# Performance work log

Hardware: AMD Instinct MI355X
Metric: run time of the kernel (lower is better)

The kernel has to match this reference:

```python
import jax, jax.numpy as jnp
import numpy as np

B = 32768   # batch
F = 32      # per-node feature dim
H = 256     # hidden width
M = 4       # modules per node
OUT = 8     # final output dim
INIT_W = 0.003
B_INIT = 0.1


def _lin(k, din, dout):
    # fanin_init-style uniform weights, bias filled with 0.1 (hidden layers)
    s = 1.0 / np.sqrt(din)
    W = jax.random.uniform(k, (M, din, dout), jnp.float32, -s, s)
    b = jnp.full((M, dout), B_INIT, jnp.float32)
    return W, b


def setup_inputs() -> dict:
    key = jax.random.key(0)
    ks = jax.random.split(key, 16)
    feats = jax.random.normal(ks[0], (B, 4 * F), jnp.float32)
    idx = jax.random.randint(ks[1], (B, 4), 0, M)
    onehots = jax.nn.one_hot(idx, M, dtype=jnp.float32).reshape(B, 4 * M)
    input_val = jnp.concatenate([feats, onehots], axis=1)  # [B,144]

    W00, b00 = _lin(ks[2], F, H)        # node0 post layer 0
    W01, b01 = _lin(ks[3], H, H)        # node0 post layer 1
    Wpre1, bpre1 = _lin(ks[4], F, H)    # node1 pre
    Wpost1, bpost1 = _lin(ks[5], 2 * H, H)  # node1 interface (prev 256 + own 256)
    Wpre2, bpre2 = _lin(ks[6], F, H)
    Wpost2, bpost2 = _lin(ks[7], 2 * H, H)
    Wpre3, bpre3 = _lin(ks[8], F, H)
    Wpost3, bpost3 = _lin(ks[9], 2 * H, H)
    # final output layer: uniform(-init_w, init_w) for W and b, identity act
    Wfin3 = jax.random.uniform(ks[10], (M, H, OUT), jnp.float32, -INIT_W, INIT_W)
    bfin3 = jax.random.uniform(ks[11], (M, OUT), jnp.float32, -INIT_W, INIT_W)
    return dict(input_val=input_val,
                W00=W00, b00=b00, W01=W01, b01=b01,
                Wpre1=Wpre1, bpre1=bpre1, Wpost1=Wpost1, bpost1=bpost1,
                Wpre2=Wpre2, bpre2=bpre2, Wpost2=Wpost2, bpost2=bpost2,
                Wpre3=Wpre3, bpre3=bpre3, Wpost3=Wpost3, bpost3=bpost3,
                Wfin3=Wfin3, bfin3=bfin3)


def _select(h, onehot):
    # per-row pick of the assigned module's output: [B,M,D],[B,M] -> [B,D]
    return jnp.einsum('bmo,bm->bo', h, onehot)


def reference(input_val, W00, b00, W01, b01,
              Wpre1, bpre1, Wpost1, bpost1,
              Wpre2, bpre2, Wpost2, bpost2,
              Wpre3, bpre3, Wpost3, bpost3,
              Wfin3, bfin3):
    feat = lambda j: input_val[:, j * F:(j + 1) * F]
    oh = lambda j: input_val[:, 4 * F + j * M: 4 * F + (j + 1) * M]

    # node 0: two hidden layers, module-dispatched (dense-all-modules + one-hot combine)
    h = jax.nn.relu(jnp.einsum('bi,mio->bmo', feat(0), W00) + b00)
    h = jax.nn.relu(jnp.einsum('bmi,mio->bmo', h, W01) + b01)
    x = _select(h, oh(0))  # [B,H]

    def node(x_prev, fj, ohj, Wpre, bpre, Wpost, bpost):
        hp = jax.nn.relu(jnp.einsum('bi,mio->bmo', fj, Wpre) + bpre)
        # interface layer consumes concat([x_prev, hp]); split the weight to
        # avoid materializing [B,M,2H]
        hq = jax.nn.relu(jnp.einsum('bi,mio->bmo', x_prev, Wpost[:, :H, :])
                         + jnp.einsum('bmi,mio->bmo', hp, Wpost[:, H:, :])
                         + bpost)
        return hq  # [B,M,H]

    x = _select(node(x, feat(1), oh(1), Wpre1, bpre1, Wpost1, bpost1), oh(1))
    x = _select(node(x, feat(2), oh(2), Wpre2, bpre2, Wpost2, bpost2), oh(2))

    h3 = node(x, feat(3), oh(3), Wpre3, bpre3, Wpost3, bpost3)  # [B,M,H]
    out = jnp.einsum('bmi,mio->bmo', h3, Wfin3) + bfin3          # final linear, identity act
    return _select(out, oh(3))  # [B,OUT]
```

## Files before the change

### kernel.cpp

```cpp
#include <hip/hip_runtime.h>

#define NB 32768
#define MAXTILE 768
#define ROWS 64
#define NT 4
#define XHS 536

typedef short s8v __attribute__((ext_vector_type(8)));
typedef short s4v __attribute__((ext_vector_type(4)));
typedef float f4v __attribute__((ext_vector_type(4)));
typedef unsigned short u16;
typedef unsigned short u16x4 __attribute__((ext_vector_type(4)));
typedef unsigned int u32;
typedef unsigned char u8;

__device__ __forceinline__ float bf2f(u16 u) { return __uint_as_float(((u32)u) << 16); }
__device__ __forceinline__ u16 f2bf(float f) {
    u32 x = __float_as_uint(f);
    x += 0x7FFFu + ((x >> 16) & 1u);
    return (u16)(x >> 16);
}
__device__ __forceinline__ s8v ld8(const u16* p) { return *reinterpret_cast<const s8v*>(p); }

#define MFMA16(a, b, c) __builtin_amdgcn_mfma_f32_16x16x32_bf16((a), (b), (c), 0, 0, 0)

template <int N> struct IC { static constexpr int v = N; };

__device__ __forceinline__ void detect_flag(const void* input, int tid, int* shflag)
{
    if (tid < 64) {
        u32 w = ((const u32*)input)[tid];
        u32 h0 = w & 0xFFFFu;
        u32 e0 = (h0 >> 7) & 0xFFu;
        bool plaus = (h0 == 0u) || (e0 >= 96u && e0 <= 143u);
        unsigned long long m = __ballot(plaus);
        if (tid == 0) *shflag = (__popcll(m) >= 48) ? 1 : 0;
    }
}

struct RepArgs {
    const void* W01; const void* Wp[3]; const void* pre[4]; const void* fin;
    const void* bias[9];
    u16 *rPre, *rW01, *rWp[3], *rFin, *cbias;
};

__global__ __launch_bounds__(256) void prepA_kernel(const void* __restrict__ inputv,
                                                    int* __restrict__ histT,
                                                    u16* __restrict__ keyloc,
                                                    RepArgs R)
{
    __shared__ int lcnt[256];
    __shared__ u16 T[2048];
    __shared__ int shmisc;
    int tid = threadIdx.x;
    int b = blockIdx.x;
    detect_flag(inputv, tid, &shmisc);
    __syncthreads();
    int flag = shmisc;

    if (b < 128) {
        lcnt[tid] = 0;
        __syncthreads();
        int row = (b << 8) + tid;
        const u32* in32 = (const u32*)inputv;
        const u16* in16 = (const u16*)inputv;
        int key = 0;
#pragma unroll
        for (int j = 0; j < 4; j++) {
            int base = row * 144 + 128 + j * 4;
            u32 v1, v2, v3;
            if (flag) { v1 = in16[base + 1]; v2 = in16[base + 2]; v3 = in16[base + 3]; }
            else      { v1 = in32[base + 1]; v2 = in32[base + 2]; v3 = in32[base + 3]; }
            int m = v1 ? 1 : (v2 ? 2 : (v3 ? 3 : 0));
            key |= m << (j << 1);
        }
        int loc = atomicAdd(&lcnt[key], 1);
        keyloc[row] = (u16)(key | (loc << 8));
        __syncthreads();
        histT[tid * 128 + b] = lcnt[tid];
        return;
    }

    int rb = b - 128;
    const void* src; u16* dst; int K, k0, mrow, kq;
    if (rb < 128) {
        int tile = rb >> 2; kq = rb & 3;
        int m = tile >> 3, s = tile & 7;
        src = R.W01; dst = R.rW01 + (m * 8 + s) * 8192; K = 256; k0 = s * 32; mrow = m;
    } else if (rb < 896) {
        int u = rb - 128, mat = u >> 8, r = u & 255;
        int tile = r >> 2; kq = r & 3;
        int m = tile >> 4, s = tile & 15;
        src = R.Wp[mat]; dst = R.rWp[mat] + (m * 16 + s) * 8192; K = 512; k0 = s * 32; mrow = m;
    } else if (rb < 960) {
        int u = rb - 896;
        int tile = u >> 2; kq = u & 3;
        int mat = tile >> 2, m = tile & 3;
        src = R.pre[mat]; dst = R.rPre + (mat * 4 + m) * 8192; K = 32; k0 = 0; mrow = m;
    } else if (rb < 964) {
        int m = rb - 960;
        const u16* s16 = (const u16*)R.fin;
        const float* s32 = (const float*)R.fin;
        u16* d = R.rFin + m * 4096;
        for (int half = 0; half < 2; half++) {
            for (int i = tid; i < 1024; i += 256) {
                int kk = half * 128 + (i >> 3);
                T[i] = flag ? s16[(m * 256 + kk) * 8 + (i & 7)]
                            : f2bf(s32[(m * 256 + kk) * 8 + (i & 7)]);
            }
            __syncthreads();
            for (int i = tid; i < 2048; i += 256) {
                int s = (half << 2) + (i >> 9), lane = (i >> 3) & 63, j = i & 7;
                int q = lane >> 4, l16 = lane & 15;
                int k = s * 32 + q * 8 + j;
                d[s * 512 + lane * 8 + j] = (l16 < 8) ? T[(k - half * 128) * 8 + l16] : (u16)0;
            }
            __syncthreads();
        }
        return;
    } else {
        const int sz[9] = {1024,1024,1024,1024,1024,1024,1024,1024,32};
        const int of[9] = {0,1024,2048,3072,4096,5120,6144,7168,8192};
        for (int i = tid; i < 8224; i += 256) {
            int t = i, e = 0;
            while (t >= sz[e]) { t -= sz[e]; e++; }
            R.cbias[of[e] + t] = flag ? ((const u16*)R.bias[e])[t]
                                      : f2bf(((const float*)R.bias[e])[t]);
        }
        return;
    }
    const u16* s16 = (const u16*)src;
    const float* s32 = (const float*)src;
    for (int i = tid; i < 2048; i += 256) {
        int kk = i >> 8, n = i & 255;
        int srcIdx = (mrow * K + k0 + kq * 8 + kk) * 256 + n;
        T[i] = flag ? s16[srcIdx] : f2bf(s32[srcIdx]);
    }
    __syncthreads();
    for (int i = tid; i < 2048; i += 256) {
        int mt = i >> 7, r = i & 127, l15 = r >> 3, j = i & 7;
        dst[mt * 512 + kq * 128 + r] = T[j * 256 + mt * 16 + l15];
    }
}

__global__ __launch_bounds__(256) void scatter_kernel(const int* __restrict__ histT,
                                                      const u16* __restrict__ keyloc,
                                                      int* __restrict__ perm,
                                                      int4* __restrict__ tileInfo)
{
    __shared__ int lcnt[256];
    __shared__ int sBase[256];
    int tid = threadIdx.x;
    int b = blockIdx.x;

    const int4* hrow = (const int4*)(histT + tid * 128);
    int tot = 0, before = 0;
#pragma unroll
    for (int j = 0; j < 32; j++) {
        int4 h = hrow[j];
        int i4 = j << 2;
        tot += h.x + h.y + h.z + h.w;
        if (i4 + 0 < b) before += h.x;
        if (i4 + 1 < b) before += h.y;
        if (i4 + 2 < b) before += h.z;
        if (i4 + 3 < b) before += h.w;
    }
    lcnt[tid] = tot;
    __syncthreads();
    for (int off = 1; off < 256; off <<= 1) {
        int v = (tid >= off) ? lcnt[tid - off] : 0;
        __syncthreads();
        lcnt[tid] += v;
        __syncthreads();
    }
    int gbase = lcnt[tid] - tot;
    sBase[tid] = gbase + before;
    __syncthreads();

    if (b == 0) {
        int tiles = (tot + ROWS - 1) / ROWS;
        lcnt[tid] = tiles;
        __syncthreads();
        for (int off = 1; off < 256; off <<= 1) {
            int v = (tid >= off) ? lcnt[tid - off] : 0;
            __syncthreads();
            lcnt[tid] += v;
            __syncthreads();
        }
        int tbase = lcnt[tid] - tiles;
        int ttot = lcnt[255];
        for (int t = 0; t < tiles; t++) {
            int rem = tot - t * ROWS;
            tileInfo[tbase + t] = make_int4(tid, gbase + t * ROWS, rem > ROWS ? ROWS : rem, 0);
        }
        for (int i = ttot + tid; i < MAXTILE; i += 256)
            tileInfo[i] = make_int4(0, 0, 0, 0);
    }

    int row = (b << 8) + tid;
    u32 kl = keyloc[row];
    int key = kl & 255, loc = kl >> 8;
    perm[sBase[key] + loc] = row;
}

struct MainP { const u16 *rPre, *rW01, *rWp1, *rWp2, *rWp3, *rFin, *cbias; };

__global__ __launch_bounds__(1024, 8) void main_kernel(
    const void* __restrict__ inRaw,
    const int* __restrict__ perm, const int4* __restrict__ tileInfo,
    MainP P, void* __restrict__ outp)
{
    __shared__ __align__(16) u16 xh[ROWS * XHS];
    __shared__ int rowids[ROWS];
    __shared__ int shflag;

    int tid = threadIdx.x;
    int lane = tid & 63, w = tid >> 6, quad = lane >> 4, l16 = lane & 15;

    int4 ti = tileInfo[blockIdx.x];
    int key = ti.x, ppos = ti.y, cntIn = ti.z;
    if (cntIn <= 0) return;

    detect_flag(inRaw, tid, &shflag);
    if (tid < ROWS) {
        int g = tid < cntIn ? tid : cntIn - 1;
        rowids[tid] = perm[ppos + g];
    }
    __syncthreads();
    int flag = shflag;
    int rows_[NT];
#pragma unroll
    for (int nt = 0; nt < NT; nt++) rows_[nt] = rowids[nt * 16 + l16];

    const u16* in16 = (const u16*)inRaw;
    const float* in32 = (const float*)inRaw;
    int mt = w;

    f4v acc[NT];
    s8v fb[NT];

    auto gemm_run = [&](auto nc, const u16* Ab, int ks0) {
        constexpr int N = decltype(nc)::v;
        constexpr int D = 3;
        const u16* base = Ab + mt * 512 + lane * 8;
        s8v A[D];
#pragma unroll
        for (int d = 0; d < D && d < N; d++) A[d] = ld8(base + d * 8192);
        __syncthreads();
#pragma unroll
        for (int s = 0; s < N; s++) {
            s8v c = A[s % D];
            if (s + D < N) A[s % D] = ld8(base + (s + D) * 8192);
#pragma unroll
            for (int nt = 0; nt < NT; nt++) {
                s8v B = ld8(&xh[(nt * 16 + l16) * XHS + (ks0 + s) * 32 + quad * 8]);
                acc[nt] = MFMA16(c, B, acc[nt]);
            }
        }
    };

    for (int node = 0; node < 4; node++) {
        int m = (key >> (node << 1)) & 3;

#pragma unroll
        for (int nt = 0; nt < NT; nt++) {
            int off = rows_[nt] * 144 + (node << 5) + (quad << 3);
            if (flag) fb[nt] = ld8(in16 + off);
            else {
                f4v f0 = *(const f4v*)(in32 + off);
                f4v f1 = *(const f4v*)(in32 + off + 4);
                s8v r;
#pragma unroll
                for (int j = 0; j < 4; j++) { r[j] = (short)f2bf(f0[j]); r[4 + j] = (short)f2bf(f1[j]); }
                fb[nt] = r;
            }
        }

        {
            const u16* preB = P.rPre + ((node << 2) + m) * 8192;
            s8v a = ld8(preB + mt * 512 + lane * 8);
            u16x4 bv = *(const u16x4*)(P.cbias + node * 2048 + m * 256 + mt * 16 + quad * 4);
            f4v bias;
#pragma unroll
            for (int r = 0; r < 4; r++) bias[r] = bf2f(bv[r]);
#pragma unroll
            for (int nt = 0; nt < NT; nt++) {
                f4v c = MFMA16(a, fb[nt], bias);
                s4v p;
#pragma unroll
                for (int r = 0; r < 4; r++) { float v = c[r] > 0.f ? c[r] : 0.f; p[r] = (short)f2bf(v); }
                *(s4v*)&xh[(nt * 16 + l16) * XHS + 256 + mt * 16 + quad * 4] = p;
            }
        }

        {
            u16x4 bv = *(const u16x4*)(P.cbias + node * 2048 + 1024 + m * 256 + mt * 16 + quad * 4);
            f4v f0;
#pragma unroll
            for (int r = 0; r < 4; r++) f0[r] = bf2f(bv[r]);
#pragma unroll
            for (int nt = 0; nt < NT; nt++) acc[nt] = f0;
        }

        if (node == 0) gemm_run(IC<8>{},  P.rW01 + m * 8 * 8192, 8);
        else {
            const u16* WB = (node == 1 ? P.rWp1 : (node == 2 ? P.rWp2 : P.rWp3)) + m * 16 * 8192;
            gemm_run(IC<16>{}, WB, 0);
        }
        __syncthreads();

#pragma unroll
        for (int nt = 0; nt < NT; nt++) {
            s4v p;
#pragma unroll
            for (int r = 0; r < 4; r++) { float v = acc[nt][r] > 0.f ? acc[nt][r] : 0.f; p[r] = (short)f2bf(v); }
            *(s4v*)&xh[(nt * 16 + l16) * XHS + mt * 16 + quad * 4] = p;
        }
    }
    __syncthreads();

    if (w < NT) {
        int m3 = (key >> 6) & 3;
        f4v c;
#pragma unroll
        for (int r = 0; r < 4; r++)
            c[r] = (quad < 2) ? bf2f(P.cbias[8192 + m3 * 8 + quad * 4 + r]) : 0.f;
#pragma unroll
        for (int s = 0; s < 8; s++) {
            s8v A = ld8(P.rFin + m3 * 4096 + s * 512 + lane * 8);
            s8v B = ld8(&xh[(w * 16 + l16) * XHS + s * 32 + quad * 8]);
            c = MFMA16(A, B, c);
        }
        int bidx = w * 16 + l16;
        if (quad < 2 && bidx < cntIn) {
            int row = rowids[bidx];
            if (flag) {
                s4v p;
#pragma unroll
                for (int r = 0; r < 4; r++) p[r] = (short)f2bf(c[r]);
                *(s4v*)((u16*)outp + row * 8 + quad * 4) = p;
            } else {
                *(f4v*)((float*)outp + row * 8 + quad * 4) = c;
            }
        }
    }
}

extern "C" void kernel_launch(void* const* d_in, const int* in_sizes, int n_in,
                              void* d_out, int out_size, void* d_ws, size_t ws_size,
                              hipStream_t stream)
{
    (void)in_sizes; (void)n_in; (void)out_size;
    const void* input  = d_in[0];
    const void* W00    = d_in[1];
    const void* b00    = d_in[2];
    const void* W01    = d_in[3];
    const void* b01    = d_in[4];
    const void* Wpre1  = d_in[5];
    const void* bpre1  = d_in[6];
    const void* Wpost1 = d_in[7];
    const void* bpost1 = d_in[8];
    const void* Wpre2  = d_in[9];
    const void* bpre2  = d_in[10];
    const void* Wpost2 = d_in[11];
    const void* bpost2 = d_in[12];
    const void* Wpre3  = d_in[13];
    const void* bpre3  = d_in[14];
    const void* Wpost3 = d_in[15];
    const void* bpost3 = d_in[16];
    const void* Wfin   = d_in[17];
    const void* bfin   = d_in[18];

    char* base = (char*)d_ws;
    size_t off = 0;
    auto alloc = [&](size_t bytes) -> char* {
        char* p = base + off;
        off += (bytes + 255) & ~(size_t)255;
        return p;
    };
    int*  histT     = (int*)alloc(256 * 128 * 4);
    u16*  keyloc    = (u16*)alloc(NB * 2);
    int4* tileInfo  = (int4*)alloc(MAXTILE * 16);
    int*  perm      = (int*)alloc((size_t)NB * 4);
    u16*  cbias    = (u16*)alloc(8224 * 2);
    u16*  rPre     = (u16*)alloc(131072 * 2);
    u16*  rW01     = (u16*)alloc(262144 * 2);
    u16*  rWp1     = (u16*)alloc(524288 * 2);
    u16*  rWp2     = (u16*)alloc(524288 * 2);
    u16*  rWp3     = (u16*)alloc(524288 * 2);
    u16*  rFin     = (u16*)alloc(16384 * 2);
    if (off > ws_size) return;

    RepArgs R;
    R.W01 = W01; R.Wp[0] = Wpost1; R.Wp[1] = Wpost2; R.Wp[2] = Wpost3;
    R.pre[0] = W00; R.pre[1] = Wpre1; R.pre[2] = Wpre2; R.pre[3] = Wpre3;
    R.fin = Wfin;
    R.bias[0] = b00;   R.bias[1] = b01;
    R.bias[2] = bpre1; R.bias[3] = bpost1;
    R.bias[4] = bpre2; R.bias[5] = bpost2;
    R.bias[6] = bpre3; R.bias[7] = bpost3;
    R.bias[8] = bfin;
    R.rPre = rPre; R.rW01 = rW01;
    R.rWp[0] = rWp1; R.rWp[1] = rWp2; R.rWp[2] = rWp3;
    R.rFin = rFin; R.cbias = cbias;

    prepA_kernel<<<1093, 256, 0, stream>>>(input, histT, keyloc, R);
    scatter_kernel<<<128, 256, 0, stream>>>(histT, keyloc, perm, tileInfo);

    MainP P;
    P.rPre = rPre; P.rW01 = rW01; P.rWp1 = rWp1; P.rWp2 = rWp2; P.rWp3 = rWp3;
    P.rFin = rFin; P.cbias = cbias;
    main_kernel<<<MAXTILE, 1024, 0, stream>>>(input, perm, tileInfo, P, d_out);
}
```

Baseline: 212.3 us.

## Compute two M-tiles per wave in 512-thread blocks with XCD-grouped tile mapping

```diff
diff --git a/kernel.cpp b/kernel.cpp
--- a/kernel.cpp
+++ b/kernel.cpp
@@ -146,7 +146,8 @@
 __global__ __launch_bounds__(256) void scatter_kernel(const int* __restrict__ histT,
                                                       const u16* __restrict__ keyloc,
                                                       int* __restrict__ perm,
-                                                      int4* __restrict__ tileInfo)
+                                                      int4* __restrict__ tileInfo,
+                                                      int* __restrict__ tcount)
 {
     __shared__ int lcnt[256];
     __shared__ int sBase[256];
@@ -189,6 +190,7 @@
         }
         int tbase = lcnt[tid] - tiles;
         int ttot = lcnt[255];
+        if (tid == 0) tcount[0] = ttot;
         for (int t = 0; t < tiles; t++) {
             int rem = tot - t * ROWS;
             tileInfo[tbase + t] = make_int4(tid, gbase + t * ROWS, rem > ROWS ? ROWS : rem, 0);
@@ -205,9 +207,10 @@
 
 struct MainP { const u16 *rPre, *rW01, *rWp1, *rWp2, *rWp3, *rFin, *cbias; };
 
-__global__ __launch_bounds__(1024, 8) void main_kernel(
+__global__ __launch_bounds__(512, 4) void main_kernel(
     const void* __restrict__ inRaw,
     const int* __restrict__ perm, const int4* __restrict__ tileInfo,
+    const int* __restrict__ tcount,
     MainP P, void* __restrict__ outp)
 {
     __shared__ __align__(16) u16 xh[ROWS * XHS];
@@ -217,7 +220,13 @@
     int tid = threadIdx.x;
     int lane = tid & 63, w = tid >> 6, quad = lane >> 4, l16 = lane & 15;
 
-    int4 ti = tileInfo[blockIdx.x];
+    int T = tcount[0];
+    int tpx = (T + 7) >> 3;
+    int x = blockIdx.x & 7, i = blockIdx.x >> 3;
+    if (i >= tpx) return;
+    int t = x * tpx + i;
+    if (t >= T) return;
+    int4 ti = tileInfo[t];
     int key = ti.x, ppos = ti.y, cntIn = ti.z;
     if (cntIn <= 0) return;
 
@@ -234,27 +243,34 @@
 
     const u16* in16 = (const u16*)inRaw;
     const float* in32 = (const float*)inRaw;
-    int mt = w;
-
-    f4v acc[NT];
-    s8v fb[NT];
+    int mt0 = w << 1, mt1 = mt0 + 1;
+
+    f4v acc0[NT], acc1[NT];
 
     auto gemm_run = [&](auto nc, const u16* Ab, int ks0) {
         constexpr int N = decltype(nc)::v;
-        constexpr int D = 3;
-        const u16* base = Ab + mt * 512 + lane * 8;
-        s8v A[D];
-#pragma unroll
-        for (int d = 0; d < D && d < N; d++) A[d] = ld8(base + d * 8192);
+        constexpr int D = 4;
+        const u16* base0 = Ab + mt0 * 512 + lane * 8;
+        const u16* base1 = Ab + mt1 * 512 + lane * 8;
+        s8v A0[D], A1[D];
+#pragma unroll
+        for (int d = 0; d < D && d < N; d++) {
+            A0[d] = ld8(base0 + d * 8192);
+            A1[d] = ld8(base1 + d * 8192);
+        }
         __syncthreads();
 #pragma unroll
         for (int s = 0; s < N; s++) {
-            s8v c = A[s % D];
-            if (s + D < N) A[s % D] = ld8(base + (s + D) * 8192);
+            s8v c0 = A0[s % D], c1 = A1[s % D];
+            if (s + D < N) {
+                A0[s % D] = ld8(base0 + (s + D) * 8192);
+                A1[s % D] = ld8(base1 + (s + D) * 8192);
+            }
 #pragma unroll
             for (int nt = 0; nt < NT; nt++) {
                 s8v B = ld8(&xh[(nt * 16 + l16) * XHS + (ks0 + s) * 32 + quad * 8]);
-                acc[nt] = MFMA16(c, B, acc[nt]);
+                acc0[nt] = MFMA16(c0, B, acc0[nt]);
+                acc1[nt] = MFMA16(c1, B, acc1[nt]);
             }
         }
     };
@@ -262,6 +278,7 @@
     for (int node = 0; node < 4; node++) {
         int m = (key >> (node << 1)) & 3;
 
+        s8v fb[NT];
 #pragma unroll
         for (int nt = 0; nt < NT; nt++) {
             int off = rows_[nt] * 144 + (node << 5) + (quad << 3);
@@ -276,8 +293,10 @@
             }
         }
 
-        {
-            const u16* preB = P.rPre + ((node << 2) + m) * 8192;
+        const u16* preB = P.rPre + ((node << 2) + m) * 8192;
+#pragma unroll
+        for (int ci = 0; ci < 2; ci++) {
+            int mt = mt0 + ci;
             s8v a = ld8(preB + mt * 512 + lane * 8);
             u16x4 bv = *(const u16x4*)(P.cbias + node * 2048 + m * 256 + mt * 16 + quad * 4);
             f4v bias;
@@ -294,12 +313,13 @@
         }
 
         {
-            u16x4 bv = *(const u16x4*)(P.cbias + node * 2048 + 1024 + m * 256 + mt * 16 + quad * 4);
-            f4v f0;
-#pragma unroll
-            for (int r = 0; r < 4; r++) f0[r] = bf2f(bv[r]);
-#pragma unroll
-            for (int nt = 0; nt < NT; nt++) acc[nt] = f0;
+            u16x4 b0 = *(const u16x4*)(P.cbias + node * 2048 + 1024 + m * 256 + mt0 * 16 + quad * 4);
+            u16x4 b1 = *(const u16x4*)(P.cbias + node * 2048 + 1024 + m * 256 + mt1 * 16 + quad * 4);
+            f4v f0, f1;
+#pragma unroll
+            for (int r = 0; r < 4; r++) { f0[r] = bf2f(b0[r]); f1[r] = bf2f(b1[r]); }
+#pragma unroll
+            for (int nt = 0; nt < NT; nt++) { acc0[nt] = f0; acc1[nt] = f1; }
         }
 
         if (node == 0) gemm_run(IC<8>{},  P.rW01 + m * 8 * 8192, 8);
@@ -310,11 +330,16 @@
         __syncthreads();
 
 #pragma unroll
-        for (int nt = 0; nt < NT; nt++) {
-            s4v p;
-#pragma unroll
-            for (int r = 0; r < 4; r++) { float v = acc[nt][r] > 0.f ? acc[nt][r] : 0.f; p[r] = (short)f2bf(v); }
-            *(s4v*)&xh[(nt * 16 + l16) * XHS + mt * 16 + quad * 4] = p;
+        for (int ci = 0; ci < 2; ci++) {
+            int mt = mt0 + ci;
+#pragma unroll
+            for (int nt = 0; nt < NT; nt++) {
+                f4v a = ci ? acc1[nt] : acc0[nt];
+                s4v p;
+#pragma unroll
+                for (int r = 0; r < 4; r++) { float v = a[r] > 0.f ? a[r] : 0.f; p[r] = (short)f2bf(v); }
+                *(s4v*)&xh[(nt * 16 + l16) * XHS + mt * 16 + quad * 4] = p;
+            }
         }
     }
     __syncthreads();
@@ -382,6 +407,7 @@
     u16*  keyloc    = (u16*)alloc(NB * 2);
     int4* tileInfo  = (int4*)alloc(MAXTILE * 16);
     int*  perm      = (int*)alloc((size_t)NB * 4);
+    int*  tcount    = (int*)alloc(4);
     u16*  cbias    = (u16*)alloc(8224 * 2);
     u16*  rPre     = (u16*)alloc(131072 * 2);
     u16*  rW01     = (u16*)alloc(262144 * 2);
@@ -405,10 +431,10 @@
     R.rFin = rFin; R.cbias = cbias;
 
     prepA_kernel<<<1093, 256, 0, stream>>>(input, histT, keyloc, R);
-    scatter_kernel<<<128, 256, 0, stream>>>(histT, keyloc, perm, tileInfo);
+    scatter_kernel<<<128, 256, 0, stream>>>(histT, keyloc, perm, tileInfo, tcount);
 
     MainP P;
     P.rPre = rPre; P.rW01 = rW01; P.rWp1 = rWp1; P.rWp2 = rWp2; P.rWp3 = rWp3;
     P.rFin = rFin; P.cbias = cbias;
-    main_kernel<<<MAXTILE, 1024, 0, stream>>>(input, perm, tileInfo, P, d_out);
-}
+    main_kernel<<<MAXTILE, 512, 0, stream>>>(input, perm, tileInfo, tcount, P, d_out);
+}
```

New measurement: 194.7 us. 1.09x faster.
